# Kernel tuning notes

Hardware: AMD Instinct MI355X
Metric: run time of the kernel (lower is better)

## Reference

```python
import jax, jax.numpy as jnp
import numpy as np

N_NODES = 50000
N_EDGES = 800000
D = 128


def setup_inputs() -> dict:
    key = jax.random.key(0)
    k1, k2, k3, k4, k5 = jax.random.split(key, 5)
    node_attr = jax.random.normal(k1, (N_NODES, D), dtype=jnp.float32)
    edge_index = jax.random.randint(k2, (2, N_EDGES), 0, N_NODES, dtype=jnp.int64)
    edge_attr = jax.random.normal(k3, (N_EDGES, D), dtype=jnp.float32)
    # 2-layer MLP: (3D -> D) -> ReLU -> (D -> D), scaled init
    w1 = jax.random.normal(k4, (3 * D, D), dtype=jnp.float32) * (1.0 / np.sqrt(3 * D))
    b1 = jnp.zeros((D,), dtype=jnp.float32)
    w2 = jax.random.normal(k5, (D, D), dtype=jnp.float32) * (1.0 / np.sqrt(D))
    b2 = jnp.zeros((D,), dtype=jnp.float32)
    return {"node_attr": node_attr, "edge_index": edge_index, "edge_attr": edge_attr,
            "w1": w1, "b1": b1, "w2": w2, "b2": b2}


def reference(node_attr, edge_index, edge_attr, w1, b1, w2, b2):
    senders_idx = edge_index[0]
    receivers_idx = edge_index[1]
    senders_attr = node_attr[senders_idx]      # [E, D] irregular gather
    receivers_attr = node_attr[receivers_idx]  # [E, D] irregular gather
    collected = jnp.concatenate([senders_attr, receivers_attr, edge_attr], axis=1)  # [E, 3D]
    h = jax.nn.relu(collected @ w1 + b1)       # [E, D]
    edge_attr_new = h @ w2 + b2                # [E, D]
    return edge_attr_new
```

## Files before the change

kernel.cpp:

```cpp
#include <hip/hip_runtime.h>


#define NE 800000
#define ND 50000
#define DD 128

typedef float f32x4v __attribute__((ext_vector_type(4)));
typedef float f32x4a __attribute__((ext_vector_type(4)));
typedef _Float16 f16x8 __attribute__((ext_vector_type(8)));
typedef _Float16 f16x4 __attribute__((ext_vector_type(4)));

__device__ __forceinline__ f16x4 cvt4(f32x4v v) {
    f16x4 r;
    r[0] = (_Float16)v[0]; r[1] = (_Float16)v[1];
    r[2] = (_Float16)v[2]; r[3] = (_Float16)v[3];
    return r;
}

__global__ void prep_w(const float* __restrict__ w1, const float* __restrict__ w2,
                       _Float16* __restrict__ w1t, _Float16* __restrict__ w2f) {
    int i = blockIdx.x * 256 + threadIdx.x;
    if (i < 384 * 128) {
        int col = i / 384;
        int k = i - col * 384;
        float v = w1[(size_t)k * 128 + col];
        int byteoff = col * 768 + ((k * 2) ^ ((col & 15) << 4));
        *(_Float16*)((char*)w1t + byteoff) = (_Float16)v;
    } else {
        int j = i - 384 * 128;
        int ks = j >> 10;
        int col = (j >> 3) & 127;
        int jj = j & 7;
        w2f[j] = (_Float16)w2[(size_t)(ks * 8 + jj) * 128 + col];
    }
}

__global__ void prep_node(const float* __restrict__ node_attr, _Float16* __restrict__ nf16) {
    int i = blockIdx.x * 256 + threadIdx.x;
    const float* src = node_attr + (size_t)i * 8;
    f32x4v a = *(const f32x4v*)src;
    f32x4v b = *(const f32x4v*)(src + 4);
    f16x8 r;
    r[0] = (_Float16)a[0]; r[1] = (_Float16)a[1];
    r[2] = (_Float16)a[2]; r[3] = (_Float16)a[3];
    r[4] = (_Float16)b[0]; r[5] = (_Float16)b[1];
    r[6] = (_Float16)b[2]; r[7] = (_Float16)b[3];
    *(f16x8*)(nf16 + (size_t)i * 8) = r;
}

#define MFMA_SEG(SEG)                                                                     \
    _Pragma("unroll")                                                                     \
    for (int kk = 0; kk < 4; kk++) {                                                      \
        f16x8 a = *(const f16x8*)(ab + r15 * 256 + ((kk * 64 + q16) ^ xa));               \
        _Pragma("unroll")                                                                 \
        for (int n = 0; n < 8; n++) {                                                     \
            const int col = n * 16 + r15;                                                 \
            f16x8 b = *(const f16x8*)(lds + col * 768 +                                   \
                       ((((SEG) * 4 + kk) * 64 + q16) ^ xa));                             \
            acc[n] = __builtin_amdgcn_mfma_f32_16x16x32_f16(a, b, acc[n], 0, 0, 0);       \
        }                                                                                 \
    }

#define WRITE_SEG16(V)                                                                    \
    _Pragma("unroll")                                                                     \
    for (int i = 0; i < 8; i++) {                                                         \
        const int row = 2 * i + sub;                                                      \
        *(f16x4*)(ab + row * 256 + ((c31 * 8) ^ ((row & 15) << 4))) = V[i];               \
    }

__global__ __attribute__((amdgpu_flat_work_group_size(768, 768),
                          amdgpu_waves_per_eu(3, 3)))
void edge_mlp(
    const float* __restrict__ node_attr,
    const int* __restrict__ eidx,
    const float* __restrict__ edge_attr,
    const _Float16* __restrict__ w1t,
    const float* __restrict__ b1,
    const _Float16* __restrict__ w2f,
    const float* __restrict__ b2,
    const _Float16* __restrict__ nf16,
    float* __restrict__ out) {
    extern __shared__ char lds[];

    const int tid = threadIdx.x;
    const int wid = tid >> 6;
    const int lane = tid & 63;
    const int r15 = lane & 15;
    const int q16 = (lane >> 4) * 16;
    const int sub = lane >> 5;
    const int c31 = lane & 31;

    {
        const char* src = (const char*)w1t;
        #pragma unroll
        for (int i = 0; i < 8; i++) {
            int off = (tid + i * 768) * 16;
            *(f16x8*)(lds + off) = *(const f16x8*)(src + off);
        }
    }

    float b1v[8], b2v[8];
    #pragma unroll
    for (int n = 0; n < 8; n++) { b1v[n] = b1[n * 16 + r15]; b2v[n] = b2[n * 16 + r15]; }

    __syncthreads();

    char* ab = lds + 96 * 1024 + wid * 4096;
    const int xa = r15 << 4;
    int ebase = blockIdx.x * 192 + wid * 16;
    if (ebase > NE - 16) ebase = NE - 16;

    const int sidx = eidx[ebase + r15];
    const int ridx = eidx[NE + ebase + r15];

    f16x4 sv[8];
    #pragma unroll
    for (int i = 0; i < 8; i++) {
        int r = __shfl(sidx, 2 * i + sub);
        sv[i] = *(const f16x4*)(nf16 + (size_t)r * DD + c31 * 4);
    }
    WRITE_SEG16(sv)

    f16x4 rv[8];
    #pragma unroll
    for (int i = 0; i < 8; i++) {
        int r = __shfl(ridx, 2 * i + sub);
        rv[i] = *(const f16x4*)(nf16 + (size_t)r * DD + c31 * 4);
    }

    f32x4a acc[8] = {};
    __builtin_amdgcn_wave_barrier();

    MFMA_SEG(0)

    WRITE_SEG16(rv)
    f32x4v ev[8];
    #pragma unroll
    for (int i = 0; i < 8; i++) {
        const int row = 2 * i + sub;
        ev[i] = __builtin_nontemporal_load(
            (const f32x4v*)(edge_attr + (size_t)(ebase + row) * DD + c31 * 4));
    }
    __builtin_amdgcn_wave_barrier();

    MFMA_SEG(1)

    #pragma unroll
    for (int i = 0; i < 8; i++) {
        const int row = 2 * i + sub;
        *(f16x4*)(ab + row * 256 + ((c31 * 8) ^ ((row & 15) << 4))) = cvt4(ev[i]);
    }
    f16x8 b2fa[2][8];
    #pragma unroll
    for (int kk = 0; kk < 2; kk++)
        #pragma unroll
        for (int n = 0; n < 8; n++) {
            const int ks = kk * 4 + (lane >> 4);
            b2fa[kk][n] = *(const f16x8*)(w2f + ((size_t)(ks * 128 + n * 16 + r15)) * 8);
        }
    __builtin_amdgcn_wave_barrier();

    MFMA_SEG(2)

    #pragma unroll
    for (int n = 0; n < 8; n++) {
        const int col = n * 16 + r15;
        #pragma unroll
        for (int reg = 0; reg < 4; reg++) {
            const int row = (lane >> 4) * 4 + reg;
            float v = fmaxf(acc[n][reg] + b1v[n], 0.0f);
            *(_Float16*)(ab + row * 256 + ((col * 2) ^ ((row & 15) << 4))) = (_Float16)v;
        }
    }
    __builtin_amdgcn_wave_barrier();

    f32x4a acc2[8] = {};
    #pragma unroll
    for (int kk = 0; kk < 2; kk++) {
        f16x8 a = *(const f16x8*)(ab + r15 * 256 + ((kk * 64 + q16) ^ xa));
        #pragma unroll
        for (int n = 0; n < 8; n++)
            acc2[n] = __builtin_amdgcn_mfma_f32_16x16x32_f16(a, b2fa[kk][n], acc2[n], 0, 0, 0);
    }
    f16x8 b2fb[2][8];
    #pragma unroll
    for (int kk = 0; kk < 2; kk++)
        #pragma unroll
        for (int n = 0; n < 8; n++) {
            const int ks = (kk + 2) * 4 + (lane >> 4);
            b2fb[kk][n] = *(const f16x8*)(w2f + ((size_t)(ks * 128 + n * 16 + r15)) * 8);
        }
    #pragma unroll
    for (int kk = 2; kk < 4; kk++) {
        f16x8 a = *(const f16x8*)(ab + r15 * 256 + ((kk * 64 + q16) ^ xa));
        #pragma unroll
        for (int n = 0; n < 8; n++)
            acc2[n] = __builtin_amdgcn_mfma_f32_16x16x32_f16(a, b2fb[kk - 2][n], acc2[n], 0, 0, 0);
    }

    #pragma unroll
    for (int n = 0; n < 8; n++) {
        #pragma unroll
        for (int reg = 0; reg < 4; reg++) {
            const int row = (lane >> 4) * 4 + reg;
            __builtin_nontemporal_store(acc2[n][reg] + b2v[n],
                out + (size_t)(ebase + row) * DD + n * 16 + r15);
        }
    }
}

extern "C" void kernel_launch(void* const* d_in, const int* in_sizes, int n_in,
                              void* d_out, int out_size, void* d_ws, size_t ws_size,
                              hipStream_t stream) {
    const float* node_attr = (const float*)d_in[0];
    const int* eidx = (const int*)d_in[1];
    const float* edge_attr = (const float*)d_in[2];
    const float* w1 = (const float*)d_in[3];
    const float* b1 = (const float*)d_in[4];
    const float* w2 = (const float*)d_in[5];
    const float* b2 = (const float*)d_in[6];
    float* out = (float*)d_out;

    _Float16* w1t = (_Float16*)d_ws;
    _Float16* w2f = w1t + 384 * 128;
    _Float16* nf16 = w2f + 128 * 128;

    hipFuncSetAttribute((const void*)edge_mlp,
                        hipFuncAttributeMaxDynamicSharedMemorySize, 160 * 1024);

    prep_w<<<256, 256, 0, stream>>>(w1, w2, w1t, w2f);
    prep_node<<<3125, 256, 0, stream>>>(node_attr, nf16);
    edge_mlp<<<4167, 768, 144 * 1024, stream>>>(node_attr, eidx, edge_attr,
                                                w1t, b1, w2f, b2, nf16, out);
}
```

Measured before the change: 242.2 us.

## Process two 16-edge tiles per wave and prefetch second tile's sender gather

Each wave now handles two consecutive 16-edge tiles, so the grid is halved and the 96KB W1 copy into LDS is amortized over twice as many edges. Edge indices for both tiles are loaded before the weight copy, and the second tile's sender-row gather is issued during the first tile's last MFMA segment, behind a sched_barrier. Output stores switch from nontemporal to ordinary stores. The extra live registers for the prefetched gather may strain the fixed 3-waves-per-EU budget, and fewer blocks means a coarser tail.

Measured after the change: 626.5 us. +158.7%, slower.

```diff
diff --git a/kernel.cpp b/kernel.cpp
--- a/kernel.cpp
+++ b/kernel.cpp
@@ -90,6 +90,14 @@
     const int sub = lane >> 5;
     const int c31 = lane & 31;
 
+    int gb = blockIdx.x * 384 + wid * 32;
+    int eb0 = gb;          if (eb0 > NE - 16) eb0 = NE - 16;
+    int eb1 = gb + 16;     if (eb1 > NE - 16) eb1 = NE - 16;
+    const int sidx0 = eidx[eb0 + r15];
+    const int ridx0 = eidx[NE + eb0 + r15];
+    const int sidx1 = eidx[eb1 + r15];
+    const int ridx1 = eidx[NE + eb1 + r15];
+
     {
         const char* src = (const char*)w1t;
         #pragma unroll
@@ -107,104 +115,195 @@
 
     char* ab = lds + 96 * 1024 + wid * 4096;
     const int xa = r15 << 4;
-    int ebase = blockIdx.x * 192 + wid * 16;
-    if (ebase > NE - 16) ebase = NE - 16;
-
-    const int sidx = eidx[ebase + r15];
-    const int ridx = eidx[NE + ebase + r15];
-
-    f16x4 sv[8];
+
+    f16x4 sv0[8];
     #pragma unroll
     for (int i = 0; i < 8; i++) {
-        int r = __shfl(sidx, 2 * i + sub);
-        sv[i] = *(const f16x4*)(nf16 + (size_t)r * DD + c31 * 4);
-    }
-    WRITE_SEG16(sv)
-
-    f16x4 rv[8];
-    #pragma unroll
-    for (int i = 0; i < 8; i++) {
-        int r = __shfl(ridx, 2 * i + sub);
-        rv[i] = *(const f16x4*)(nf16 + (size_t)r * DD + c31 * 4);
-    }
-
-    f32x4a acc[8] = {};
-    __builtin_amdgcn_wave_barrier();
-
-    MFMA_SEG(0)
-
-    WRITE_SEG16(rv)
-    f32x4v ev[8];
-    #pragma unroll
-    for (int i = 0; i < 8; i++) {
-        const int row = 2 * i + sub;
-        ev[i] = __builtin_nontemporal_load(
-            (const f32x4v*)(edge_attr + (size_t)(ebase + row) * DD + c31 * 4));
-    }
-    __builtin_amdgcn_wave_barrier();
-
-    MFMA_SEG(1)
-
-    #pragma unroll
-    for (int i = 0; i < 8; i++) {
-        const int row = 2 * i + sub;
-        *(f16x4*)(ab + row * 256 + ((c31 * 8) ^ ((row & 15) << 4))) = cvt4(ev[i]);
-    }
-    f16x8 b2fa[2][8];
-    #pragma unroll
-    for (int kk = 0; kk < 2; kk++)
+        int r = __shfl(sidx0, 2 * i + sub);
+        sv0[i] = *(const f16x4*)(nf16 + (size_t)r * DD + c31 * 4);
+    }
+    f16x4 sv1[8];
+
+    {
+        const int ebase = eb0;
+        WRITE_SEG16(sv0)
+
+        f16x4 rv[8];
+        #pragma unroll
+        for (int i = 0; i < 8; i++) {
+            int r = __shfl(ridx0, 2 * i + sub);
+            rv[i] = *(const f16x4*)(nf16 + (size_t)r * DD + c31 * 4);
+        }
+
+        f32x4a acc[8] = {};
+        __builtin_amdgcn_wave_barrier();
+        MFMA_SEG(0)
+
+        WRITE_SEG16(rv)
+        f32x4v ev[8];
+        #pragma unroll
+        for (int i = 0; i < 8; i++) {
+            const int row = 2 * i + sub;
+            ev[i] = __builtin_nontemporal_load(
+                (const f32x4v*)(edge_attr + (size_t)(ebase + row) * DD + c31 * 4));
+        }
+        __builtin_amdgcn_wave_barrier();
+        MFMA_SEG(1)
+
+        #pragma unroll
+        for (int i = 0; i < 8; i++) {
+            const int row = 2 * i + sub;
+            *(f16x4*)(ab + row * 256 + ((c31 * 8) ^ ((row & 15) << 4))) = cvt4(ev[i]);
+        }
+        f16x8 b2fa[2][8];
+        #pragma unroll
+        for (int kk = 0; kk < 2; kk++)
+            #pragma unroll
+            for (int n = 0; n < 8; n++) {
+                const int ks = kk * 4 + (lane >> 4);
+                b2fa[kk][n] = *(const f16x8*)(w2f + ((size_t)(ks * 128 + n * 16 + r15)) * 8);
+            }
+        #pragma unroll
+        for (int i = 0; i < 8; i++) {
+            int r = __shfl(sidx1, 2 * i + sub);
+            sv1[i] = *(const f16x4*)(nf16 + (size_t)r * DD + c31 * 4);
+        }
+        __builtin_amdgcn_sched_barrier(0);
+        __builtin_amdgcn_wave_barrier();
+        MFMA_SEG(2)
+
         #pragma unroll
         for (int n = 0; n < 8; n++) {
-            const int ks = kk * 4 + (lane >> 4);
-            b2fa[kk][n] = *(const f16x8*)(w2f + ((size_t)(ks * 128 + n * 16 + r15)) * 8);
-        }
-    __builtin_amdgcn_wave_barrier();
-
-    MFMA_SEG(2)
-
-    #pragma unroll
-    for (int n = 0; n < 8; n++) {
-        const int col = n * 16 + r15;
-        #pragma unroll
-        for (int reg = 0; reg < 4; reg++) {
-            const int row = (lane >> 4) * 4 + reg;
-            float v = fmaxf(acc[n][reg] + b1v[n], 0.0f);
-            *(_Float16*)(ab + row * 256 + ((col * 2) ^ ((row & 15) << 4))) = (_Float16)v;
-        }
-    }
-    __builtin_amdgcn_wave_barrier();
-
-    f32x4a acc2[8] = {};
-    #pragma unroll
-    for (int kk = 0; kk < 2; kk++) {
-        f16x8 a = *(const f16x8*)(ab + r15 * 256 + ((kk * 64 + q16) ^ xa));
-        #pragma unroll
-        for (int n = 0; n < 8; n++)
-            acc2[n] = __builtin_amdgcn_mfma_f32_16x16x32_f16(a, b2fa[kk][n], acc2[n], 0, 0, 0);
-    }
-    f16x8 b2fb[2][8];
-    #pragma unroll
-    for (int kk = 0; kk < 2; kk++)
+            const int col = n * 16 + r15;
+            #pragma unroll
+            for (int reg = 0; reg < 4; reg++) {
+                const int row = (lane >> 4) * 4 + reg;
+                float v = fmaxf(acc[n][reg] + b1v[n], 0.0f);
+                *(_Float16*)(ab + row * 256 + ((col * 2) ^ ((row & 15) << 4))) = (_Float16)v;
+            }
+        }
+        __builtin_amdgcn_wave_barrier();
+
+        f32x4a acc2[8] = {};
+        #pragma unroll
+        for (int kk = 0; kk < 2; kk++) {
+            f16x8 a = *(const f16x8*)(ab + r15 * 256 + ((kk * 64 + q16) ^ xa));
+            #pragma unroll
+            for (int n = 0; n < 8; n++)
+                acc2[n] = __builtin_amdgcn_mfma_f32_16x16x32_f16(a, b2fa[kk][n], acc2[n], 0, 0, 0);
+        }
+        f16x8 b2fb[2][8];
+        #pragma unroll
+        for (int kk = 0; kk < 2; kk++)
+            #pragma unroll
+            for (int n = 0; n < 8; n++) {
+                const int ks = (kk + 2) * 4 + (lane >> 4);
+                b2fb[kk][n] = *(const f16x8*)(w2f + ((size_t)(ks * 128 + n * 16 + r15)) * 8);
+            }
+        #pragma unroll
+        for (int kk = 2; kk < 4; kk++) {
+            f16x8 a = *(const f16x8*)(ab + r15 * 256 + ((kk * 64 + q16) ^ xa));
+            #pragma unroll
+            for (int n = 0; n < 8; n++)
+                acc2[n] = __builtin_amdgcn_mfma_f32_16x16x32_f16(a, b2fb[kk - 2][n], acc2[n], 0, 0, 0);
+        }
+
         #pragma unroll
         for (int n = 0; n < 8; n++) {
-            const int ks = (kk + 2) * 4 + (lane >> 4);
-            b2fb[kk][n] = *(const f16x8*)(w2f + ((size_t)(ks * 128 + n * 16 + r15)) * 8);
-        }
-    #pragma unroll
-    for (int kk = 2; kk < 4; kk++) {
-        f16x8 a = *(const f16x8*)(ab + r15 * 256 + ((kk * 64 + q16) ^ xa));
-        #pragma unroll
-        for (int n = 0; n < 8; n++)
-            acc2[n] = __builtin_amdgcn_mfma_f32_16x16x32_f16(a, b2fb[kk - 2][n], acc2[n], 0, 0, 0);
-    }
-
-    #pragma unroll
-    for (int n = 0; n < 8; n++) {
-        #pragma unroll
-        for (int reg = 0; reg < 4; reg++) {
-            const int row = (lane >> 4) * 4 + reg;
-            __builtin_nontemporal_store(acc2[n][reg] + b2v[n],
-                out + (size_t)(ebase + row) * DD + n * 16 + r15);
+            #pragma unroll
+            for (int reg = 0; reg < 4; reg++) {
+                const int row = (lane >> 4) * 4 + reg;
+                out[(size_t)(ebase + row) * DD + n * 16 + r15] = acc2[n][reg] + b2v[n];
+            }
+        }
+    }
+
+    {
+        const int ebase = eb1;
+        __builtin_amdgcn_wave_barrier();
+        WRITE_SEG16(sv1)
+
+        f16x4 rv[8];
+        #pragma unroll
+        for (int i = 0; i < 8; i++) {
+            int r = __shfl(ridx1, 2 * i + sub);
+            rv[i] = *(const f16x4*)(nf16 + (size_t)r * DD + c31 * 4);
+        }
+
+        f32x4a acc[8] = {};
+        __builtin_amdgcn_wave_barrier();
+        MFMA_SEG(0)
+
+        WRITE_SEG16(rv)
+        f32x4v ev[8];
+        #pragma unroll
+        for (int i = 0; i < 8; i++) {
+            const int row = 2 * i + sub;
+            ev[i] = __builtin_nontemporal_load(
+                (const f32x4v*)(edge_attr + (size_t)(ebase + row) * DD + c31 * 4));
+        }
+        __builtin_amdgcn_wave_barrier();
+        MFMA_SEG(1)
+
+        #pragma unroll
+        for (int i = 0; i < 8; i++) {
+            const int row = 2 * i + sub;
+            *(f16x4*)(ab + row * 256 + ((c31 * 8) ^ ((row & 15) << 4))) = cvt4(ev[i]);
+        }
+        f16x8 b2fa[2][8];
+        #pragma unroll
+        for (int kk = 0; kk < 2; kk++)
+            #pragma unroll
+            for (int n = 0; n < 8; n++) {
+                const int ks = kk * 4 + (lane >> 4);
+                b2fa[kk][n] = *(const f16x8*)(w2f + ((size_t)(ks * 128 + n * 16 + r15)) * 8);
+            }
+        __builtin_amdgcn_wave_barrier();
+        MFMA_SEG(2)
+
+        #pragma unroll
+        for (int n = 0; n < 8; n++) {
+            const int col = n * 16 + r15;
+            #pragma unroll
+            for (int reg = 0; reg < 4; reg++) {
+                const int row = (lane >> 4) * 4 + reg;
+                float v = fmaxf(acc[n][reg] + b1v[n], 0.0f);
+                *(_Float16*)(ab + row * 256 + ((col * 2) ^ ((row & 15) << 4))) = (_Float16)v;
+            }
+        }
+        __builtin_amdgcn_wave_barrier();
+
+        f32x4a acc2[8] = {};
+        #pragma unroll
+        for (int kk = 0; kk < 2; kk++) {
+            f16x8 a = *(const f16x8*)(ab + r15 * 256 + ((kk * 64 + q16) ^ xa));
+            #pragma unroll
+            for (int n = 0; n < 8; n++)
+                acc2[n] = __builtin_amdgcn_mfma_f32_16x16x32_f16(a, b2fa[kk][n], acc2[n], 0, 0, 0);
+        }
+        f16x8 b2fb[2][8];
+        #pragma unroll
+        for (int kk = 0; kk < 2; kk++)
+            #pragma unroll
+            for (int n = 0; n < 8; n++) {
+                const int ks = (kk + 2) * 4 + (lane >> 4);
+                b2fb[kk][n] = *(const f16x8*)(w2f + ((size_t)(ks * 128 + n * 16 + r15)) * 8);
+            }
+        #pragma unroll
+        for (int kk = 2; kk < 4; kk++) {
+            f16x8 a = *(const f16x8*)(ab + r15 * 256 + ((kk * 64 + q16) ^ xa));
+            #pragma unroll
+            for (int n = 0; n < 8; n++)
+                acc2[n] = __builtin_amdgcn_mfma_f32_16x16x32_f16(a, b2fb[kk - 2][n], acc2[n], 0, 0, 0);
+        }
+
+        #pragma unroll
+        for (int n = 0; n < 8; n++) {
+            #pragma unroll
+            for (int reg = 0; reg < 4; reg++) {
+                const int row = (lane >> 4) * 4 + reg;
+                out[(size_t)(ebase + row) * DD + n * 16 + r15] = acc2[n][reg] + b2v[n];
+            }
         }
     }
 }
@@ -230,6 +329,6 @@
 
     prep_w<<<256, 256, 0, stream>>>(w1, w2, w1t, w2f);
     prep_node<<<3125, 256, 0, stream>>>(node_attr, nf16);
-    edge_mlp<<<4167, 768, 144 * 1024, stream>>>(node_attr, eidx, edge_attr,
+    edge_mlp<<<2084, 768, 144 * 1024, stream>>>(node_attr, eidx, edge_attr,
                                                 w1t, b1, w2f, b2, nf16, out);
 }
```
